# Kernel tuning notes

Hardware: AMD Instinct MI355X
Metric: run time of the kernel (lower is better)

## Reference

```python
import jax, jax.numpy as jnp
import numpy as np

# ---- static radial-binning geometry for a 64x64 grid (classic azimuthalAverage) ----
_N = 64
_yy, _xx = np.indices((_N, _N))
_cx = (_xx.max() - _xx.min()) / 2.0  # 31.5
_cy = (_yy.max() - _yy.min()) / 2.0  # 31.5
_r = np.hypot(_xx - _cx, _yy - _cy)
_rint = _r.astype(int).ravel()                 # (4096,) integer radius per pixel
_NBINS = int(_rint.max()) + 1                  # 45 distinct integer radii (0..44)
_counts = np.bincount(_rint, minlength=_NBINS).astype(np.float32)
# classic azimuthalAverage (cumsum-of-sorted trick) returns bins 1 .. NBINS-2 inclusive
_ONEHOT = jnp.asarray(np.eye(_NBINS, dtype=np.float32)[_rint])  # (4096, 45) scatter matrix
_NR = jnp.asarray(_counts[1:_NBINS - 1])       # (43,) pixels per returned bin


def _tke(x):
    # x: (B, T, 2, 64, 64) -> turbulent kinetic energy (B, 64, 64)
    x = x.reshape(x.shape[0], -1, 2, _N, _N)
    mean_flow = jnp.mean(x, axis=1, keepdims=True)
    tur = jnp.mean((x - mean_flow) ** 2, axis=1)   # (B, 2, 64, 64) per-component variance
    return (tur[:, 0] + tur[:, 1]) * 0.5


def _spectrum(x):
    # TKE -> 2D power spectrum -> radial (azimuthal) average, all batched.
    tke = _tke(x)
    sp = jnp.fft.fftshift(jnp.fft.fft2(tke), axes=(-2, -1))
    power = jnp.real(sp * jnp.conj(sp)).reshape(x.shape[0], -1)  # (B, 4096)
    sums = power @ _ONEHOT                          # (B, 45) per-integer-radius sums
    return sums[:, 1:_NBINS - 1] / _NR              # (B, 43) azimuthal average


def setup_inputs() -> dict:
    key = jax.random.key(0)
    k1, k2 = jax.random.split(key)
    preds = jax.random.normal(k1, (64, 60, 2, 64, 64), dtype=jnp.float32)
    trues = jax.random.normal(k2, (64, 60, 2, 64, 64), dtype=jnp.float32)
    return {"preds": preds, "trues": trues}


def reference(preds, trues):
    # SpectrumLoss with loss = MSE: loss(tke2spectrum(trues), tke2spectrum(preds))
    sp_t = _spectrum(trues)
    sp_p = _spectrum(preds)
    return jnp.mean((sp_t - sp_p) ** 2)
```

## Files before the change

### kernel.cpp

```cpp
#include <hip/hip_runtime.h>
#include <math.h>

#define TT 60
#define BB 64
#define STR 68
#define NBINS 45

typedef float f32x4 __attribute__((ext_vector_type(4)));

__global__ __launch_bounds__(256) void tke_kernel(const float* __restrict__ preds,
                                                  const float* __restrict__ trues,
                                                  float* __restrict__ tke) {
    int gtid  = blockIdx.x * 256 + threadIdx.x;
    int input = gtid >> 16;
    int rem   = gtid & 65535;
    int b     = rem >> 10;
    int p4    = rem & 1023;

    const f32x4* src  = (const f32x4*)(input ? trues : preds);
    const f32x4* base = src + (size_t)b * (TT * 2048) + p4;

    float su[4]  = {0, 0, 0, 0}, squ[4] = {0, 0, 0, 0};
    float sv[4]  = {0, 0, 0, 0}, sqv[4] = {0, 0, 0, 0};
    #pragma unroll 4
    for (int t = 0; t < TT; ++t) {
        f32x4 u = __builtin_nontemporal_load(base + t * 2048);
        f32x4 v = __builtin_nontemporal_load(base + t * 2048 + 1024);
        #pragma unroll
        for (int j = 0; j < 4; ++j) {
            float uu = u[j], vv = v[j];
            su[j]  += uu;  squ[j] += uu * uu;
            sv[j]  += vv;  sqv[j] += vv * vv;
        }
    }
    const float inv = 1.0f / 60.0f;
    float o[4];
    #pragma unroll
    for (int j = 0; j < 4; ++j) {
        float mu = su[j] * inv, mv = sv[j] * inv;
        o[j] = 0.5f * ((squ[j] * inv - mu * mu) + (sqv[j] * inv - mv * mv));
    }
    float4 outv; outv.x = o[0]; outv.y = o[1]; outv.z = o[2]; outv.w = o[3];
    ((float4*)tke)[(size_t)(input * BB + b) * 1024 + p4] = outv;
}

__global__ __launch_bounds__(512) void dft_kernel(const float* __restrict__ tke,
                                                  float* __restrict__ binsums) {
    __shared__ __align__(16) float tke_s[64 * 64];
    __shared__ __align__(16) float Gr[64 * STR];
    __shared__ __align__(16) float Gi[64 * STR];
    __shared__ float ctab[64], stab[64];
    __shared__ float bins_s[NBINS];

    int tid = threadIdx.x;
    int img = blockIdx.x;

    if (tid < 64) {
        float ang = (float)tid * 0.09817477042468103871f;
        float ss, cc;
        sincosf(ang, &ss, &cc);
        ctab[tid] = cc; stab[tid] = ss;
    }
    if (tid < NBINS) bins_s[tid] = 0.0f;

    {
        const float4* src = (const float4*)(tke + (size_t)img * 4096);
        float4* dst = (float4*)tke_s;
        for (int i = tid; i < 1024; i += 512) dst[i] = src[i];
    }
    __syncthreads();

    {
        int k  = tid >> 3;
        int x0 = (tid & 7) * 8;
        float gr[8] = {0,0,0,0,0,0,0,0};
        float gi[8] = {0,0,0,0,0,0,0,0};
        for (int y = 0; y < 64; ++y) {
            float4 ta = *(const float4*)&tke_s[(y << 6) + x0];
            float4 tb = *(const float4*)&tke_s[(y << 6) + x0 + 4];
            float tv[8] = {ta.x, ta.y, ta.z, ta.w, tb.x, tb.y, tb.z, tb.w};
            int idx = (k * y) & 63;
            float cc = ctab[idx], ss = stab[idx];
            #pragma unroll
            for (int j = 0; j < 8; ++j) {
                gr[j] += cc * tv[j];
                gi[j] -= ss * tv[j];
            }
        }
        #pragma unroll
        for (int j = 0; j < 8; ++j) {
            Gr[(x0 + j) * STR + k] = gr[j];
            Gi[(x0 + j) * STR + k] = gi[j];
        }
    }
    __syncthreads();

    {
        int l  = tid >> 3;
        int k0 = (tid & 7) * 8;
        float fr[8] = {0,0,0,0,0,0,0,0};
        float fi[8] = {0,0,0,0,0,0,0,0};
        for (int x = 0; x < 64; ++x) {
            float4 a0 = *(const float4*)&Gr[x * STR + k0];
            float4 a1 = *(const float4*)&Gr[x * STR + k0 + 4];
            float4 b0 = *(const float4*)&Gi[x * STR + k0];
            float4 b1 = *(const float4*)&Gi[x * STR + k0 + 4];
            float ar[8] = {a0.x, a0.y, a0.z, a0.w, a1.x, a1.y, a1.z, a1.w};
            float br[8] = {b0.x, b0.y, b0.z, b0.w, b1.x, b1.y, b1.z, b1.w};
            int idx = (l * x) & 63;
            float cc = ctab[idx], ss = stab[idx];
            #pragma unroll
            for (int j = 0; j < 8; ++j) {
                fr[j] += ar[j] * cc + br[j] * ss;
                fi[j] += br[j] * cc - ar[j] * ss;
            }
        }
        float fl = (float)((l + 32) & 63) - 31.5f;
        #pragma unroll
        for (int j = 0; j < 8; ++j) {
            int k = k0 + j;
            float fk = (float)((k + 32) & 63) - 31.5f;
            float r = sqrtf(fk * fk + fl * fl);
            int bin = (int)r;
            float pw = fr[j] * fr[j] + fi[j] * fi[j];
            atomicAdd(&bins_s[bin], pw);
        }
    }
    __syncthreads();
    if (tid < NBINS) binsums[img * NBINS + tid] = bins_s[tid];
}

__global__ __launch_bounds__(256) void loss_kernel(const float* __restrict__ binsums,
                                                   float* __restrict__ out) {
    __shared__ int   cnt[NBINS];
    __shared__ float part[256];
    int tid = threadIdx.x;
    if (tid < NBINS) cnt[tid] = 0;
    __syncthreads();
    for (int p = tid; p < 4096; p += 256) {
        float dy = (float)(p >> 6) - 31.5f;
        float dx = (float)(p & 63) - 31.5f;
        int bin = (int)sqrtf(dy * dy + dx * dx);
        atomicAdd(&cnt[bin], 1);
    }
    __syncthreads();
    float acc = 0.0f;
    for (int j = tid; j < BB * 43; j += 256) {
        int b   = j / 43;
        int bin = j - b * 43 + 1;
        float n  = (float)cnt[bin];
        float st = binsums[(BB + b) * NBINS + bin] / n;
        float sp = binsums[b * NBINS + bin] / n;
        float d  = st - sp;
        acc += d * d;
    }
    part[tid] = acc;
    __syncthreads();
    for (int s = 128; s > 0; s >>= 1) {
        if (tid < s) part[tid] += part[tid + s];
        __syncthreads();
    }
    if (tid == 0) out[0] = part[0] * (1.0f / (BB * 43.0f));
}

extern "C" void kernel_launch(void* const* d_in, const int* in_sizes, int n_in,
                              void* d_out, int out_size, void* d_ws, size_t ws_size,
                              hipStream_t stream) {
    const float* preds = (const float*)d_in[0];
    const float* trues = (const float*)d_in[1];
    float* tke     = (float*)d_ws;
    float* binsums = tke + 2 * BB * 4096;

    tke_kernel<<<512, 256, 0, stream>>>(preds, trues, tke);
    dft_kernel<<<128, 512, 0, stream>>>(tke, binsums);
    loss_kernel<<<1, 256, 0, stream>>>(binsums, (float*)d_out);
}
```

Measured before the change: 71.99 us.

## Stream TKE loads through a 4-slot LDS ring with async global_load_lds

Reworks the memory-bound TKE reduction so each wave issues asynchronous global-to-LDS loads (global_load_lds) into a 4-deep ring buffer. It waits on vmcnt before consuming each slot, which keeps several timesteps of loads in flight while the accumulation runs. The accumulators are also switched to 4-wide vector types. This trades the nontemporal register loads for an LDS round-trip and hand-written waitcnt scheduling, so its benefit depends on whether the deeper prefetch raises achieved HBM bandwidth.

```diff
diff --git a/kernel.cpp b/kernel.cpp
--- a/kernel.cpp
+++ b/kernel.cpp
@@ -11,35 +11,64 @@
 __global__ __launch_bounds__(256) void tke_kernel(const float* __restrict__ preds,
                                                   const float* __restrict__ trues,
                                                   float* __restrict__ tke) {
-    int gtid  = blockIdx.x * 256 + threadIdx.x;
-    int input = gtid >> 16;
-    int rem   = gtid & 65535;
-    int b     = rem >> 10;
-    int p4    = rem & 1023;
-
-    const f32x4* src  = (const f32x4*)(input ? trues : preds);
-    const f32x4* base = src + (size_t)b * (TT * 2048) + p4;
-
-    float su[4]  = {0, 0, 0, 0}, squ[4] = {0, 0, 0, 0};
-    float sv[4]  = {0, 0, 0, 0}, sqv[4] = {0, 0, 0, 0};
+    __shared__ __align__(16) float lds[4][2][1024];
+
+    int tid   = threadIdx.x;
+    int bid   = blockIdx.x;
+    int input = bid >> 8;
+    int rem   = bid & 255;
+    int b     = rem >> 2;
+    int win   = rem & 3;
+    int p4    = win * 256 + tid;
+
+    const float* src   = input ? trues : preds;
+    const float* gbase = src + (size_t)b * (TT * 8192) + (size_t)p4 * 4;
+
+    int wave_off = (tid >> 6) << 8;
+
+#define STAGE(SLOT, T) do {                                                           \
+    const float* _gu = gbase + (size_t)(T) * 8192;                                    \
+    __builtin_amdgcn_global_load_lds(_gu,        &lds[SLOT][0][wave_off], 16, 0, 0);  \
+    __builtin_amdgcn_global_load_lds(_gu + 4096, &lds[SLOT][1][wave_off], 16, 0, 0);  \
+} while (0)
+
+#define WAITSB(N) do {                                                                \
+    asm volatile("s_waitcnt vmcnt(" #N ")" ::: "memory");                             \
+    __builtin_amdgcn_sched_barrier(0);                                                \
+} while (0)
+
+#define CONSUME(SLOT) do {                                                            \
+    f32x4 u = *(const f32x4*)&lds[SLOT][0][tid * 4];                                  \
+    f32x4 v = *(const f32x4*)&lds[SLOT][1][tid * 4];                                  \
+    su += u; squ += u * u;                                                            \
+    sv += v; sqv += v * v;                                                            \
+} while (0)
+
+    f32x4 su  = {0, 0, 0, 0}, squ = {0, 0, 0, 0};
+    f32x4 sv  = {0, 0, 0, 0}, sqv = {0, 0, 0, 0};
+
+    STAGE(0, 0);
+    STAGE(1, 1);
+    STAGE(2, 2);
     #pragma unroll 4
-    for (int t = 0; t < TT; ++t) {
-        f32x4 u = __builtin_nontemporal_load(base + t * 2048);
-        f32x4 v = __builtin_nontemporal_load(base + t * 2048 + 1024);
-        #pragma unroll
-        for (int j = 0; j < 4; ++j) {
-            float uu = u[j], vv = v[j];
-            su[j]  += uu;  squ[j] += uu * uu;
-            sv[j]  += vv;  sqv[j] += vv * vv;
-        }
-    }
+    for (int t = 0; t < 56; ++t) {
+        STAGE((t + 3) & 3, t + 3);
+        WAITSB(6);
+        CONSUME(t & 3);
+    }
+    STAGE(3, 59);
+    WAITSB(6);  CONSUME(0);
+    WAITSB(4);  CONSUME(1);
+    WAITSB(2);  CONSUME(2);
+    WAITSB(0);  CONSUME(3);
+
+#undef STAGE
+#undef WAITSB
+#undef CONSUME
+
     const float inv = 1.0f / 60.0f;
-    float o[4];
-    #pragma unroll
-    for (int j = 0; j < 4; ++j) {
-        float mu = su[j] * inv, mv = sv[j] * inv;
-        o[j] = 0.5f * ((squ[j] * inv - mu * mu) + (sqv[j] * inv - mv * mv));
-    }
+    f32x4 mu = su * inv, mv = sv * inv;
+    f32x4 o  = 0.5f * ((squ * inv - mu * mu) + (sqv * inv - mv * mv));
     float4 outv; outv.x = o[0]; outv.y = o[1]; outv.z = o[2]; outv.w = o[3];
     ((float4*)tke)[(size_t)(input * BB + b) * 1024 + p4] = outv;
 }
```

Measured after the change: 70.43 us. 1.02x faster.
